# Performance work log

Measured on AMD Instinct MI355X. Metric: run time of the kernel, lower is better.

Reference implementation:

```python
import jax, jax.numpy as jnp
import numpy as np

E = 2048        # embedding_dim
H = 16          # num_q_heads
G = 4           # group_size
HKV = H // G    # num_kv_heads = 4
D = E // H      # q_head_dim = 128
KVD = E // G    # kv_head_dim = 512
B, N = 2, 2048


def setup_inputs() -> dict:
    key = jax.random.key(0)
    ks = jax.random.split(key, 5)
    s = 0.02
    return {
        "x": jax.random.normal(ks[0], (B, N, E), jnp.float32),
        "Wq": jax.random.normal(ks[1], (E, E), jnp.float32) * s,
        "Wk": jax.random.normal(ks[2], (KVD, E), jnp.float32) * s,
        "Wv": jax.random.normal(ks[3], (KVD, E), jnp.float32) * s,
        "Wo": jax.random.normal(ks[4], (E, E), jnp.float32) * s,
    }


def reference(x, Wq, Wk, Wv, Wo):
    b, n, _ = x.shape
    # projections (nn.Linear: y = x @ W.T)
    q = x @ Wq.T                              # (b, n, E)
    k = x @ Wk.T                              # (b, n, KVD)
    v = x @ Wv.T                              # (b, n, KVD)
    # split heads: q -> b h n d with h=H, then (h g) -> g,h layout
    q = q.reshape(b, n, H, D).transpose(0, 2, 1, 3)          # b H n d
    q = q.reshape(b, HKV, G, n, D).transpose(0, 2, 1, 3, 4)  # b g h n d  (h=HKV)
    k = k.reshape(b, n, HKV, D).transpose(0, 2, 1, 3)        # b h s d
    v = v.reshape(b, n, HKV, D).transpose(0, 2, 1, 3)        # b h s d
    scale = 1.0 / jnp.sqrt(jnp.asarray(D, x.dtype))
    scores = jnp.einsum('bghnd,bhsd->bghns', q, k) * scale   # full score tensor
    scores = jax.nn.softmax(scores, axis=-1)
    # dropout p=0.0 -> identity
    o = jnp.einsum('bghns,bhsd->bghnd', scores, v)           # b g h n d
    # rearrange 'b g h n d -> b n (h g) d' then concat heads
    o = o.transpose(0, 3, 2, 1, 4).reshape(b, n, E)          # b n (h g) d -> b n E
    return o @ Wo.T
```

## Files before the change

kernel.cpp:

```cpp
#include <hip/hip_runtime.h>
#include <hip/hip_bf16.h>
#include <cstdint>
#include <cstddef>

using u16 = unsigned short;
typedef __bf16 bf16x8 __attribute__((ext_vector_type(8)));
typedef float f32x4 __attribute__((ext_vector_type(4)));
typedef float f32x16 __attribute__((ext_vector_type(16)));
typedef u16 u16x4 __attribute__((ext_vector_type(4)));
typedef u16 u16x8 __attribute__((ext_vector_type(8)));
typedef uint32_t u32x4 __attribute__((ext_vector_type(4)));

__device__ __forceinline__ u16 f2bf(float f) {
  uint32_t u = __builtin_bit_cast(uint32_t, f);
  u += 0x7FFFu + ((u >> 16) & 1u);
  return (u16)(u >> 16);
}

__device__ __forceinline__ void gld_lds16(const void* g, void* l) {
  __builtin_amdgcn_global_load_lds(
      (const __attribute__((address_space(1))) unsigned int*)g,
      (__attribute__((address_space(3))) unsigned int*)l, 16, 0, 0);
}

#define MFMA16(a, b, c) __builtin_amdgcn_mfma_f32_16x16x32_bf16((a), (b), (c), 0, 0, 0)
#define MFMA32(a, b, c) __builtin_amdgcn_mfma_f32_32x32x16_bf16((a), (b), (c), 0, 0, 0)

__device__ __forceinline__ uint32_t pkbf(float a, float b) {
  uint32_t d;
  asm("v_cvt_pk_bf16_f32 %0, %1, %2" : "=v"(d) : "v"(a), "v"(b));
  return d;
}
__device__ __forceinline__ void swap32(uint32_t& a, uint32_t& b) {
  asm volatile("v_permlane32_swap_b32 %0, %1" : "+v"(a), "+v"(b));
}

__global__ void cvt_kernel(const float* __restrict__ in, u16* __restrict__ out, int n4) {
  int i = blockIdx.x * blockDim.x + threadIdx.x;
  int stride = gridDim.x * blockDim.x;
  for (; i < n4; i += stride) {
    float4 v = reinterpret_cast<const float4*>(in)[i];
    u16x4 o;
    o[0] = f2bf(v.x); o[1] = f2bf(v.y); o[2] = f2bf(v.z); o[3] = f2bf(v.w);
    reinterpret_cast<u16x4*>(out)[i] = o;
  }
}

__global__ void cvt4_kernel(const float* __restrict__ x, const float* __restrict__ Wq,
                            const float* __restrict__ Wk, const float* __restrict__ Wv,
                            u16* __restrict__ xb, u16* __restrict__ Wc) {
  int i = blockIdx.x * blockDim.x + threadIdx.x;
  int stride = gridDim.x * blockDim.x;
  for (; i < 3670016; i += stride) {
    const float* src; u16* dst; int off;
    if (i < 2097152)      { src = x;  dst = xb;            off = i; }
    else if (i < 3145728) { src = Wq; dst = Wc;            off = i - 2097152; }
    else if (i < 3407872) { src = Wk; dst = Wc + 4194304;  off = i - 3145728; }
    else                  { src = Wv; dst = Wc + 5242880;  off = i - 3407872; }
    float4 v = reinterpret_cast<const float4*>(src)[off];
    u16x4 o;
    o[0] = f2bf(v.x); o[1] = f2bf(v.y); o[2] = f2bf(v.z); o[3] = f2bf(v.w);
    reinterpret_cast<u16x4*>(dst)[off] = o;
  }
}

template <bool OUT_BF16>
__global__ __launch_bounds__(256) void gemm_bt(const u16* __restrict__ A,
                                               const u16* __restrict__ B,
                                               void* __restrict__ Cv,
                                               int M, int N, int K) {
  __shared__ __align__(16) u16 Ash[3][128 * 32];
  __shared__ __align__(16) u16 Bsh[3][128 * 32];
  const int tid = threadIdx.x;
  const int w = tid >> 6, lane = tid & 63, ql = lane & 15, g = lane >> 4;
  const int wr = w >> 1, wc = w & 1;
  const int m0 = blockIdx.y * 128, n0 = blockIdx.x * 128;
  const int srow = w * 16 + (lane >> 2);
  const int sk = (lane & 3) * 8;
  const u16* Abase = A + (size_t)(m0 + srow) * K + sk;
  const u16* Bbase = B + (size_t)(n0 + srow) * K + sk;

  f32x4 acc[4][4];
#pragma unroll
  for (int i = 0; i < 4; i++)
#pragma unroll
    for (int j = 0; j < 4; j++) acc[i][j] = f32x4{0.f, 0.f, 0.f, 0.f};

  auto stage = [&](int bi, int tile) {
    const int kt = tile * 32;
    gld_lds16(Abase + kt,                  &Ash[bi][w * 512]);
    gld_lds16(Abase + (size_t)64 * K + kt, &Ash[bi][2048 + w * 512]);
    gld_lds16(Bbase + kt,                  &Bsh[bi][w * 512]);
    gld_lds16(Bbase + (size_t)64 * K + kt, &Bsh[bi][2048 + w * 512]);
  };

  const int nt = K >> 5;
  stage(0, 0);
  stage(1, 1);
  asm volatile("s_waitcnt vmcnt(4)" ::: "memory");
  __builtin_amdgcn_sched_barrier(0);
  __builtin_amdgcn_s_barrier();
  __builtin_amdgcn_sched_barrier(0);

  int cur = 0;
  for (int t = 0; t < nt; ++t) {
    if (t + 2 < nt) {
      int stg = cur + 2; if (stg >= 3) stg -= 3;
      stage(stg, t + 2);
    }
    bf16x8 af[4], bfr[4];
#pragma unroll
    for (int i = 0; i < 4; i++)
      af[i] = *reinterpret_cast<const bf16x8*>(&Ash[cur][(wr * 64 + i * 16 + ql) * 32 + g * 8]);
#pragma unroll
    for (int j = 0; j < 4; j++)
      bfr[j] = *reinterpret_cast<const bf16x8*>(&Bsh[cur][(wc * 64 + j * 16 + ql) * 32 + g * 8]);
    __builtin_amdgcn_s_setprio(1);
#pragma unroll
    for (int i = 0; i < 4; i++)
#pragma unroll
      for (int j = 0; j < 4; j++)
        acc[i][j] = MFMA16(af[i], bfr[j], acc[i][j]);
    __builtin_amdgcn_s_setprio(0);
    if (t + 1 < nt) {
      if (t + 2 < nt) {
        asm volatile("s_waitcnt vmcnt(4)" ::: "memory");
      } else {
        asm volatile("s_waitcnt vmcnt(0)" ::: "memory");
      }
      __builtin_amdgcn_sched_barrier(0);
      __builtin_amdgcn_s_barrier();
      __builtin_amdgcn_sched_barrier(0);
    }
    cur = (cur == 2) ? 0 : cur + 1;
  }

#pragma unroll
  for (int i = 0; i < 4; i++)
#pragma unroll
    for (int j = 0; j < 4; j++)
#pragma unroll
      for (int r = 0; r < 4; r++) {
        const int row = m0 + wr * 64 + i * 16 + g * 4 + r;
        const int col = n0 + wc * 64 + j * 16 + ql;
        if constexpr (OUT_BF16)
          ((u16*)Cv)[(size_t)row * N + col] = f2bf(acc[i][j][r]);
        else
          ((float*)Cv)[(size_t)row * N + col] = acc[i][j][r];
      }
}

__global__ __launch_bounds__(256, 2) void attn_kernel(const u16* __restrict__ QKV,
                                                      u16* __restrict__ O) {
  __shared__ __align__(16) u16 Kb[2][64 * 128];
  __shared__ __align__(16) u16 Vb[3][2][128 * 32];
  const int tid = threadIdx.x, w = tid >> 6, lane = tid & 63;
  const int lq = lane & 31, hi = lane >> 5;
  const int bid = blockIdx.x;
  const int swz = (bid & 7) * 64 + (bid >> 3);
  const int qt = swz & 15;
  const int bh = swz >> 4;
  const int b = bh >> 4, h = bh & 15, hkv = h >> 2;
  const size_t rowb = (size_t)b * 2048;
  const int qbase = qt * 128 + w * 32;

  const u16* Kg = QKV + 2048 + hkv * 128;
  const u16* Vg = QKV + 2560 + hkv * 128;

  bf16x8 bq[8];
  {
    const u16* qp = QKV + (rowb + qbase + lq) * 3072 + h * 128 + hi * 8;
#pragma unroll
    for (int s5 = 0; s5 < 8; s5++)
      bq[s5] = *reinterpret_cast<const bf16x8*>(qp + s5 * 16);
  }

  const int dg = tid & 7, sl = tid >> 3;

  f32x16 oacc[4], lacc;
#pragma unroll
  for (int dt = 0; dt < 4; dt++)
#pragma unroll
    for (int i = 0; i < 16; i++) oacc[dt][i] = 0.f;
#pragma unroll
  for (int i = 0; i < 16; i++) lacc[i] = 0.f;
  float m = -INFINITY;
  const float CEXP = 0.08838834764831845f * 1.4426950408889634f;

  const bf16x8 ones = __builtin_bit_cast(bf16x8,
      u32x4{0x3F803F80u, 0x3F803F80u, 0x3F803F80u, 0x3F803F80u});

  auto stageK = [&](int pb2, int sbase) {
#pragma unroll
    for (int p = 0; p < 4; p++) {
      const int L = p * 2048 + tid * 8;
      const int s = L >> 7;
      const int gI = (L >> 3) & 15;
      gld_lds16(Kg + (rowb + sbase + s) * 3072 + ((gI ^ (s & 7)) << 3),
                &Kb[pb2][p * 2048 + w * 512]);
    }
  };
  auto writeV = [&](int vb3, const u16x8& a00, const u16x8& a01,
                    const u16x8& a10, const u16x8& a11) {
#pragma unroll
    for (int sh2 = 0; sh2 < 2; sh2++)
#pragma unroll
      for (int hf = 0; hf < 2; hf++) {
        const u16x8 v = sh2 ? (hf ? a11 : a10) : (hf ? a01 : a00);
#pragma unroll
        for (int j = 0; j < 8; j++) {
          const int d = dg * 16 + hf * 8 + j;
          const int key = ((d >> 1) ^ (d >> 4)) & 3;
          Vb[vb3][sh2][d * 32 + (sl ^ (key << 3))] = v[j];
        }
      }
  };

#define KFRAG(PB, SH, S5) \
  (*reinterpret_cast<const bf16x8*>(&Kb[PB][((SH)*32 + lq) * 128 + ((((S5)*2 + hi) ^ (lq & 7)) << 3)]))
#define VFRAG(VB, DT, SS) \
  (*reinterpret_cast<const bf16x8*>(&Vb[VB][(SS) >> 1][((DT)*32 + lq) * 32 + \
      ((((SS) & 1) * 16 + hi * 8) ^ (((((DT)*32 + lq) >> 1) ^ (((DT)*32 + lq) >> 4)) & 3) << 3)]))

  u16x8 v00, v01, v10, v11;
  {
    const u16* vp = Vg + (rowb + sl) * 3072 + dg * 16;
    v00 = *reinterpret_cast<const u16x8*>(vp);
    v01 = *reinterpret_cast<const u16x8*>(vp + 8);
    const u16* vp2 = vp + (size_t)32 * 3072;
    v10 = *reinterpret_cast<const u16x8*>(vp2);
    v11 = *reinterpret_cast<const u16x8*>(vp2 + 8);
  }
  stageK(0, 0);
  writeV(0, v00, v01, v10, v11);
  __syncthreads();

  bf16x8 pf0, pf1, pf2, pf3;
  int vprev = 2, vcur = 0, vnext = 1;

#pragma unroll 1
  for (int sb = 0; sb < 32; sb++) {
    const int pb = sb & 1;
    if (sb < 31) {
      const u16* vp = Vg + (rowb + (sb + 1) * 64 + sl) * 3072 + dg * 16;
      v00 = *reinterpret_cast<const u16x8*>(vp);
      v01 = *reinterpret_cast<const u16x8*>(vp + 8);
      const u16* vp2 = vp + (size_t)32 * 3072;
      v10 = *reinterpret_cast<const u16x8*>(vp2);
      v11 = *reinterpret_cast<const u16x8*>(vp2 + 8);
      stageK(pb ^ 1, (sb + 1) * 64);
    }

    f32x16 sc0, sc1;
#pragma unroll
    for (int i = 0; i < 16; i++) { sc0[i] = 0.f; sc1[i] = 0.f; }
    __builtin_amdgcn_s_setprio(1);
#pragma unroll
    for (int s5 = 0; s5 < 8; s5++) {
      sc0 = MFMA32(KFRAG(pb, 0, s5), bq[s5], sc0);
      sc1 = MFMA32(KFRAG(pb, 1, s5), bq[s5], sc1);
    }
    __builtin_amdgcn_s_setprio(0);

    if (sb) {
      __builtin_amdgcn_s_setprio(1);
#pragma unroll
      for (int dt = 0; dt < 4; dt++) {
        oacc[dt] = MFMA32(VFRAG(vprev, dt, 0), pf0, oacc[dt]);
        oacc[dt] = MFMA32(VFRAG(vprev, dt, 1), pf1, oacc[dt]);
        oacc[dt] = MFMA32(VFRAG(vprev, dt, 2), pf2, oacc[dt]);
        oacc[dt] = MFMA32(VFRAG(vprev, dt, 3), pf3, oacc[dt]);
      }
      __builtin_amdgcn_s_setprio(0);
    }

    float u[16];
#pragma unroll
    for (int i = 0; i < 16; i++) u[i] = fmaxf(sc0[i], sc1[i]);
#pragma unroll
    for (int i = 0; i < 8; i++) u[i] = fmaxf(u[i], u[i + 8]);
#pragma unroll
    for (int i = 0; i < 4; i++) u[i] = fmaxf(u[i], u[i + 4]);
    float mx = fmaxf(fmaxf(u[0], u[1]), fmaxf(u[2], u[3]));
    mx = fmaxf(mx, __shfl_xor(mx, 32));

    if (__any((mx - m) * CEXP > 8.0f)) {
      const float mn = fmaxf(m, mx);
      const float corr = exp2f((m - mn) * CEXP);
#pragma unroll
      for (int i = 0; i < 16; i++) lacc[i] *= corr;
#pragma unroll
      for (int dt = 0; dt < 4; dt++)
#pragma unroll
        for (int i = 0; i < 16; i++) oacc[dt][i] *= corr;
      m = mn;
    }

    const float mC = m * CEXP;
    float e0[16], e1[16];
#pragma unroll
    for (int i = 0; i < 16; i++) {
      e0[i] = exp2f(fmaf(sc0[i], CEXP, -mC));
      e1[i] = exp2f(fmaf(sc1[i], CEXP, -mC));
    }
    {
      uint32_t a, bw;
      u32x4 f;
      a = pkbf(e0[0], e0[1]);  bw = pkbf(e0[4], e0[5]);  swap32(a, bw);
      f[0] = a; f[2] = bw;
      a = pkbf(e0[2], e0[3]);  bw = pkbf(e0[6], e0[7]);  swap32(a, bw);
      f[1] = a; f[3] = bw;
      pf0 = __builtin_bit_cast(bf16x8, f);
      a = pkbf(e0[8], e0[9]);  bw = pkbf(e0[12], e0[13]); swap32(a, bw);
      f[0] = a; f[2] = bw;
      a = pkbf(e0[10], e0[11]); bw = pkbf(e0[14], e0[15]); swap32(a, bw);
      f[1] = a; f[3] = bw;
      pf1 = __builtin_bit_cast(bf16x8, f);
      a = pkbf(e1[0], e1[1]);  bw = pkbf(e1[4], e1[5]);  swap32(a, bw);
      f[0] = a; f[2] = bw;
      a = pkbf(e1[2], e1[3]);  bw = pkbf(e1[6], e1[7]);  swap32(a, bw);
      f[1] = a; f[3] = bw;
      pf2 = __builtin_bit_cast(bf16x8, f);
      a = pkbf(e1[8], e1[9]);  bw = pkbf(e1[12], e1[13]); swap32(a, bw);
      f[0] = a; f[2] = bw;
      a = pkbf(e1[10], e1[11]); bw = pkbf(e1[14], e1[15]); swap32(a, bw);
      f[1] = a; f[3] = bw;
      pf3 = __builtin_bit_cast(bf16x8, f);
    }

    lacc = MFMA32(ones, pf0, lacc);
    lacc = MFMA32(ones, pf1, lacc);
    lacc = MFMA32(ones, pf2, lacc);
    lacc = MFMA32(ones, pf3, lacc);

    if (sb < 31) writeV(vnext, v00, v01, v10, v11);
    __syncthreads();

    const int tmp = vprev; vprev = vcur; vcur = vnext; vnext = tmp;
  }

  {
    __builtin_amdgcn_s_setprio(1);
#pragma unroll
    for (int dt = 0; dt < 4; dt++) {
      oacc[dt] = MFMA32(VFRAG(vprev, dt, 0), pf0, oacc[dt]);
      oacc[dt] = MFMA32(VFRAG(vprev, dt, 1), pf1, oacc[dt]);
      oacc[dt] = MFMA32(VFRAG(vprev, dt, 2), pf2, oacc[dt]);
      oacc[dt] = MFMA32(VFRAG(vprev, dt, 3), pf3, oacc[dt]);
    }
    __builtin_amdgcn_s_setprio(0);
  }
  __syncthreads();

  const float rl = 1.0f / lacc[0];
  u16* ob = (w < 2) ? &Kb[w][0] : &Vb[w - 2][0][0];
#pragma unroll
  for (int dt = 0; dt < 4; dt++)
#pragma unroll
    for (int rq = 0; rq < 4; rq++) {
      u16x4 pv;
#pragma unroll
      for (int k = 0; k < 4; k++) pv[k] = f2bf(oacc[dt][rq * 4 + k] * rl);
      *reinterpret_cast<u16x4*>(&ob[lq * 136 + dt * 32 + rq * 8 + hi * 4]) = pv;
    }
  const int orow = lane >> 1, och = (lane & 1) * 64;
  u16* og = O + (rowb + qbase + orow) * 2048 + h * 128 + och;
#pragma unroll
  for (int t = 0; t < 8; t++) {
    u16x8 v = *reinterpret_cast<const u16x8*>(&ob[orow * 136 + och + t * 8]);
    *reinterpret_cast<u16x8*>(og + t * 8) = v;
  }
#undef KFRAG
#undef VFRAG
}

extern "C" void kernel_launch(void* const* d_in, const int* in_sizes, int n_in,
                              void* d_out, int out_size, void* d_ws, size_t ws_size,
                              hipStream_t stream) {
  (void)in_sizes; (void)n_in; (void)out_size;
  const float* x  = (const float*)d_in[0];
  const float* Wq = (const float*)d_in[1];
  const float* Wk = (const float*)d_in[2];
  const float* Wv = (const float*)d_in[3];
  const float* Wo = (const float*)d_in[4];

  if (ws_size < (size_t)(8388608 + 6291456 + 12582912) * 2) return;
  u16* xb  = (u16*)d_ws;
  u16* Wc  = xb + 8388608;
  u16* QKV = Wc + 6291456;
  u16* Ob  = xb;

  cvt4_kernel<<<2048, 256, 0, stream>>>(x, Wq, Wk, Wv, xb, Wc);
  gemm_bt<true><<<dim3(24, 32), 256, 0, stream>>>(xb, Wc, (void*)QKV, 4096, 3072, 2048);
  cvt_kernel<<<2048, 256, 0, stream>>>(Wo, Wc, 1048576);
  attn_kernel<<<dim3(512), 256, 0, stream>>>(QKV, Ob);
  gemm_bt<false><<<dim3(16, 32), 256, 0, stream>>>(Ob, Wc, d_out, 4096, 2048, 2048);
}
```

Measured before the change: 233.2 us.

## Process two query tiles per wave with 32-key blocks in attention

Each wave now owns 64 query rows, held as two 32-row MFMA tiles. Every K and V fragment read from shared memory therefore feeds two MFMAs, which halves LDS traffic per FLOP and halves the grid to 256 blocks. Key blocks shrink to 32 with plain double buffering instead of the three-stage V pipeline. The row sum is now taken with a shuffle reduction instead of an MFMA against a vector of ones. The cost is higher register pressure, fewer blocks (256 on a device with about 256 CUs), and less overlap because P·V is no longer deferred to the next iteration.

```diff
diff --git a/kernel.cpp b/kernel.cpp
--- a/kernel.cpp
+++ b/kernel.cpp
@@ -152,103 +152,86 @@
 
 __global__ __launch_bounds__(256, 2) void attn_kernel(const u16* __restrict__ QKV,
                                                       u16* __restrict__ O) {
-  __shared__ __align__(16) u16 Kb[2][64 * 128];
-  __shared__ __align__(16) u16 Vb[3][2][128 * 32];
+  __shared__ __align__(16) u16 SH[17408];
   const int tid = threadIdx.x, w = tid >> 6, lane = tid & 63;
   const int lq = lane & 31, hi = lane >> 5;
   const int bid = blockIdx.x;
-  const int swz = (bid & 7) * 64 + (bid >> 3);
-  const int qt = swz & 15;
-  const int bh = swz >> 4;
-  const int b = bh >> 4, h = bh & 15, hkv = h >> 2;
+  const int cls = bid & 7, uu = bid >> 3;
+  const int b = cls >> 2, hkv = cls & 3;
+  const int h = hkv * 4 + (uu >> 3), qt = uu & 7;
   const size_t rowb = (size_t)b * 2048;
-  const int qbase = qt * 128 + w * 32;
+  const int qbase = qt * 256 + w * 64;
 
   const u16* Kg = QKV + 2048 + hkv * 128;
   const u16* Vg = QKV + 2560 + hkv * 128;
 
-  bf16x8 bq[8];
+  bf16x8 bq0[8], bq1[8];
   {
-    const u16* qp = QKV + (rowb + qbase + lq) * 3072 + h * 128 + hi * 8;
-#pragma unroll
-    for (int s5 = 0; s5 < 8; s5++)
-      bq[s5] = *reinterpret_cast<const bf16x8*>(qp + s5 * 16);
+    const u16* qp0 = QKV + (rowb + qbase + lq) * 3072 + h * 128 + hi * 8;
+    const u16* qp1 = qp0 + (size_t)32 * 3072;
+#pragma unroll
+    for (int s5 = 0; s5 < 8; s5++) {
+      bq0[s5] = *reinterpret_cast<const bf16x8*>(qp0 + s5 * 16);
+      bq1[s5] = *reinterpret_cast<const bf16x8*>(qp1 + s5 * 16);
+    }
   }
 
   const int dg = tid & 7, sl = tid >> 3;
-
-  f32x16 oacc[4], lacc;
+  const int ks = tid >> 4, kslot = tid & 15;
+
+  f32x16 oa0[4], oa1[4];
 #pragma unroll
   for (int dt = 0; dt < 4; dt++)
 #pragma unroll
-    for (int i = 0; i < 16; i++) oacc[dt][i] = 0.f;
-#pragma unroll
-  for (int i = 0; i < 16; i++) lacc[i] = 0.f;
-  float m = -INFINITY;
+    for (int i = 0; i < 16; i++) { oa0[dt][i] = 0.f; oa1[dt][i] = 0.f; }
+  float m0 = -INFINITY, m1 = -INFINITY, l0 = 0.f, l1 = 0.f;
   const float CEXP = 0.08838834764831845f * 1.4426950408889634f;
 
-  const bf16x8 ones = __builtin_bit_cast(bf16x8,
-      u32x4{0x3F803F80u, 0x3F803F80u, 0x3F803F80u, 0x3F803F80u});
-
-  auto stageK = [&](int pb2, int sbase) {
-#pragma unroll
-    for (int p = 0; p < 4; p++) {
-      const int L = p * 2048 + tid * 8;
-      const int s = L >> 7;
-      const int gI = (L >> 3) & 15;
-      gld_lds16(Kg + (rowb + sbase + s) * 3072 + ((gI ^ (s & 7)) << 3),
-                &Kb[pb2][p * 2048 + w * 512]);
+  auto stageK = [&](int pb, int sbase) {
+#pragma unroll
+    for (int p = 0; p < 2; p++) {
+      const int s = p * 16 + ks;
+      gld_lds16(Kg + (rowb + sbase + s) * 3072 + ((kslot ^ (s & 7)) << 3),
+                &SH[pb * 4096 + p * 2048 + w * 512]);
     }
   };
-  auto writeV = [&](int vb3, const u16x8& a00, const u16x8& a01,
-                    const u16x8& a10, const u16x8& a11) {
-#pragma unroll
-    for (int sh2 = 0; sh2 < 2; sh2++)
-#pragma unroll
-      for (int hf = 0; hf < 2; hf++) {
-        const u16x8 v = sh2 ? (hf ? a11 : a10) : (hf ? a01 : a00);
-#pragma unroll
-        for (int j = 0; j < 8; j++) {
-          const int d = dg * 16 + hf * 8 + j;
-          const int key = ((d >> 1) ^ (d >> 4)) & 3;
-          Vb[vb3][sh2][d * 32 + (sl ^ (key << 3))] = v[j];
-        }
-      }
+  auto writeV = [&](int pb, const u16x8& a0, const u16x8& a1) {
+#pragma unroll
+    for (int hf = 0; hf < 2; hf++) {
+      const u16x8 v = hf ? a1 : a0;
+#pragma unroll
+      for (int j = 0; j < 8; j++) {
+        const int d = dg * 16 + hf * 8 + j;
+        const int key = ((d >> 1) ^ (d >> 4)) & 3;
+        SH[8192 + pb * 4096 + d * 32 + (sl ^ (key << 3))] = v[j];
+      }
+    }
   };
 
-#define KFRAG(PB, SH, S5) \
-  (*reinterpret_cast<const bf16x8*>(&Kb[PB][((SH)*32 + lq) * 128 + ((((S5)*2 + hi) ^ (lq & 7)) << 3)]))
-#define VFRAG(VB, DT, SS) \
-  (*reinterpret_cast<const bf16x8*>(&Vb[VB][(SS) >> 1][((DT)*32 + lq) * 32 + \
-      ((((SS) & 1) * 16 + hi * 8) ^ (((((DT)*32 + lq) >> 1) ^ (((DT)*32 + lq) >> 4)) & 3) << 3)]))
-
-  u16x8 v00, v01, v10, v11;
+#define KFRAG(PB, S5) \
+  (*reinterpret_cast<const bf16x8*>(&SH[(PB)*4096 + lq * 128 + ((((S5)*2 + hi) ^ (lq & 7)) << 3)]))
+#define VFRAG(PB, DT, SS) \
+  (*reinterpret_cast<const bf16x8*>(&SH[8192 + (PB)*4096 + ((DT)*32 + lq) * 32 + \
+      (((SS)*16 + hi * 8) ^ ((((((DT)*32 + lq) >> 1) ^ (((DT)*32 + lq) >> 4)) & 3) << 3))]))
+
+  u16x8 va, vb2;
   {
     const u16* vp = Vg + (rowb + sl) * 3072 + dg * 16;
-    v00 = *reinterpret_cast<const u16x8*>(vp);
-    v01 = *reinterpret_cast<const u16x8*>(vp + 8);
-    const u16* vp2 = vp + (size_t)32 * 3072;
-    v10 = *reinterpret_cast<const u16x8*>(vp2);
-    v11 = *reinterpret_cast<const u16x8*>(vp2 + 8);
+    va  = *reinterpret_cast<const u16x8*>(vp);
+    vb2 = *reinterpret_cast<const u16x8*>(vp + 8);
   }
   stageK(0, 0);
-  writeV(0, v00, v01, v10, v11);
+  writeV(0, va, vb2);
   __syncthreads();
 
-  bf16x8 pf0, pf1, pf2, pf3;
-  int vprev = 2, vcur = 0, vnext = 1;
-
 #pragma unroll 1
-  for (int sb = 0; sb < 32; sb++) {
+  for (int sb = 0; sb < 64; sb++) {
     const int pb = sb & 1;
-    if (sb < 31) {
-      const u16* vp = Vg + (rowb + (sb + 1) * 64 + sl) * 3072 + dg * 16;
-      v00 = *reinterpret_cast<const u16x8*>(vp);
-      v01 = *reinterpret_cast<const u16x8*>(vp + 8);
-      const u16* vp2 = vp + (size_t)32 * 3072;
-      v10 = *reinterpret_cast<const u16x8*>(vp2);
-      v11 = *reinterpret_cast<const u16x8*>(vp2 + 8);
-      stageK(pb ^ 1, (sb + 1) * 64);
+    if (sb < 63) {
+      const u16* vp = Vg + (rowb + (sb + 1) * 32 + sl) * 3072 + dg * 16;
+      va  = *reinterpret_cast<const u16x8*>(vp);
+      vb2 = *reinterpret_cast<const u16x8*>(vp + 8);
+      stageK(pb ^ 1, (sb + 1) * 32);
     }
 
     f32x16 sc0, sc1;
@@ -257,118 +240,150 @@
     __builtin_amdgcn_s_setprio(1);
 #pragma unroll
     for (int s5 = 0; s5 < 8; s5++) {
-      sc0 = MFMA32(KFRAG(pb, 0, s5), bq[s5], sc0);
-      sc1 = MFMA32(KFRAG(pb, 1, s5), bq[s5], sc1);
+      bf16x8 kf = KFRAG(pb, s5);
+      sc0 = MFMA32(kf, bq0[s5], sc0);
+      sc1 = MFMA32(kf, bq1[s5], sc1);
     }
     __builtin_amdgcn_s_setprio(0);
 
-    if (sb) {
-      __builtin_amdgcn_s_setprio(1);
-#pragma unroll
-      for (int dt = 0; dt < 4; dt++) {
-        oacc[dt] = MFMA32(VFRAG(vprev, dt, 0), pf0, oacc[dt]);
-        oacc[dt] = MFMA32(VFRAG(vprev, dt, 1), pf1, oacc[dt]);
-        oacc[dt] = MFMA32(VFRAG(vprev, dt, 2), pf2, oacc[dt]);
-        oacc[dt] = MFMA32(VFRAG(vprev, dt, 3), pf3, oacc[dt]);
-      }
-      __builtin_amdgcn_s_setprio(0);
-    }
-
-    float u[16];
-#pragma unroll
-    for (int i = 0; i < 16; i++) u[i] = fmaxf(sc0[i], sc1[i]);
-#pragma unroll
-    for (int i = 0; i < 8; i++) u[i] = fmaxf(u[i], u[i + 8]);
-#pragma unroll
-    for (int i = 0; i < 4; i++) u[i] = fmaxf(u[i], u[i + 4]);
-    float mx = fmaxf(fmaxf(u[0], u[1]), fmaxf(u[2], u[3]));
-    mx = fmaxf(mx, __shfl_xor(mx, 32));
-
-    if (__any((mx - m) * CEXP > 8.0f)) {
-      const float mn = fmaxf(m, mx);
-      const float corr = exp2f((m - mn) * CEXP);
-#pragma unroll
-      for (int i = 0; i < 16; i++) lacc[i] *= corr;
-#pragma unroll
-      for (int dt = 0; dt < 4; dt++)
-#pragma unroll
-        for (int i = 0; i < 16; i++) oacc[dt][i] *= corr;
-      m = mn;
-    }
-
-    const float mC = m * CEXP;
-    float e0[16], e1[16];
-#pragma unroll
-    for (int i = 0; i < 16; i++) {
-      e0[i] = exp2f(fmaf(sc0[i], CEXP, -mC));
-      e1[i] = exp2f(fmaf(sc1[i], CEXP, -mC));
-    }
+    bf16x8 pf00, pf01, pf10, pf11;
+
     {
-      uint32_t a, bw;
-      u32x4 f;
-      a = pkbf(e0[0], e0[1]);  bw = pkbf(e0[4], e0[5]);  swap32(a, bw);
+      float u[8];
+#pragma unroll
+      for (int i = 0; i < 8; i++) u[i] = fmaxf(sc0[i], sc0[i + 8]);
+#pragma unroll
+      for (int i = 0; i < 4; i++) u[i] = fmaxf(u[i], u[i + 4]);
+      float mx = fmaxf(fmaxf(u[0], u[1]), fmaxf(u[2], u[3]));
+      mx = fmaxf(mx, __shfl_xor(mx, 32));
+      if (__any((mx - m0) * CEXP > 8.0f)) {
+        const float mn = fmaxf(m0, mx);
+        const float corr = exp2f((m0 - mn) * CEXP);
+        l0 *= corr;
+#pragma unroll
+        for (int dt = 0; dt < 4; dt++)
+#pragma unroll
+          for (int i = 0; i < 16; i++) oa0[dt][i] *= corr;
+        m0 = mn;
+      }
+      const float mC = m0 * CEXP;
+#pragma unroll
+      for (int i = 0; i < 16; i++) sc0[i] = exp2f(fmaf(sc0[i], CEXP, -mC));
+      float s[8];
+#pragma unroll
+      for (int i = 0; i < 8; i++) s[i] = sc0[i] + sc0[i + 8];
+#pragma unroll
+      for (int i = 0; i < 4; i++) s[i] = s[i] + s[i + 4];
+      float ps = (s[0] + s[1]) + (s[2] + s[3]);
+      ps += __shfl_xor(ps, 32);
+      l0 += ps;
+      uint32_t a, bw; u32x4 f;
+      a = pkbf(sc0[0], sc0[1]);   bw = pkbf(sc0[4], sc0[5]);   swap32(a, bw);
       f[0] = a; f[2] = bw;
-      a = pkbf(e0[2], e0[3]);  bw = pkbf(e0[6], e0[7]);  swap32(a, bw);
+      a = pkbf(sc0[2], sc0[3]);   bw = pkbf(sc0[6], sc0[7]);   swap32(a, bw);
       f[1] = a; f[3] = bw;
-      pf0 = __builtin_bit_cast(bf16x8, f);
-      a = pkbf(e0[8], e0[9]);  bw = pkbf(e0[12], e0[13]); swap32(a, bw);
+      pf00 = __builtin_bit_cast(bf16x8, f);
+      a = pkbf(sc0[8], sc0[9]);   bw = pkbf(sc0[12], sc0[13]); swap32(a, bw);
       f[0] = a; f[2] = bw;
-      a = pkbf(e0[10], e0[11]); bw = pkbf(e0[14], e0[15]); swap32(a, bw);
+      a = pkbf(sc0[10], sc0[11]); bw = pkbf(sc0[14], sc0[15]); swap32(a, bw);
       f[1] = a; f[3] = bw;
-      pf1 = __builtin_bit_cast(bf16x8, f);
-      a = pkbf(e1[0], e1[1]);  bw = pkbf(e1[4], e1[5]);  swap32(a, bw);
+      pf01 = __builtin_bit_cast(bf16x8, f);
+    }
+    {
+      float u[8];
+#pragma unroll
+      for (int i = 0; i < 8; i++) u[i] = fmaxf(sc1[i], sc1[i + 8]);
+#pragma unroll
+      for (int i = 0; i < 4; i++) u[i] = fmaxf(u[i], u[i + 4]);
+      float mx = fmaxf(fmaxf(u[0], u[1]), fmaxf(u[2], u[3]));
+      mx = fmaxf(mx, __shfl_xor(mx, 32));
+      if (__any((mx - m1) * CEXP > 8.0f)) {
+        const float mn = fmaxf(m1, mx);
+        const float corr = exp2f((m1 - mn) * CEXP);
+        l1 *= corr;
+#pragma unroll
+        for (int dt = 0; dt < 4; dt++)
+#pragma unroll
+          for (int i = 0; i < 16; i++) oa1[dt][i] *= corr;
+        m1 = mn;
+      }
+      const float mC = m1 * CEXP;
+#pragma unroll
+      for (int i = 0; i < 16; i++) sc1[i] = exp2f(fmaf(sc1[i], CEXP, -mC));
+      float s[8];
+#pragma unroll
+      for (int i = 0; i < 8; i++) s[i] = sc1[i] + sc1[i + 8];
+#pragma unroll
+      for (int i = 0; i < 4; i++) s[i] = s[i] + s[i + 4];
+      float ps = (s[0] + s[1]) + (s[2] + s[3]);
+      ps += __shfl_xor(ps, 32);
+      l1 += ps;
+      uint32_t a, bw; u32x4 f;
+      a = pkbf(sc1[0], sc1[1]);   bw = pkbf(sc1[4], sc1[5]);   swap32(a, bw);
       f[0] = a; f[2] = bw;
-      a = pkbf(e1[2], e1[3]);  bw = pkbf(e1[6], e1[7]);  swap32(a, bw);
+      a = pkbf(sc1[2], sc1[3]);   bw = pkbf(sc1[6], sc1[7]);   swap32(a, bw);
       f[1] = a; f[3] = bw;
-      pf2 = __builtin_bit_cast(bf16x8, f);
-      a = pkbf(e1[8], e1[9]);  bw = pkbf(e1[12], e1[13]); swap32(a, bw);
+      pf10 = __builtin_bit_cast(bf16x8, f);
+      a = pkbf(sc1[8], sc1[9]);   bw = pkbf(sc1[12], sc1[13]); swap32(a, bw);
       f[0] = a; f[2] = bw;
-      a = pkbf(e1[10], e1[11]); bw = pkbf(e1[14], e1[15]); swap32(a, bw);
+      a = pkbf(sc1[10], sc1[11]); bw = pkbf(sc1[14], sc1[15]); swap32(a, bw);
       f[1] = a; f[3] = bw;
-      pf3 = __builtin_bit_cast(bf16x8, f);
-    }
-
-    lacc = MFMA32(ones, pf0, lacc);
-    lacc = MFMA32(ones, pf1, lacc);
-    lacc = MFMA32(ones, pf2, lacc);
-    lacc = MFMA32(ones, pf3, lacc);
-
-    if (sb < 31) writeV(vnext, v00, v01, v10, v11);
+      pf11 = __builtin_bit_cast(bf16x8, f);
+    }
+
+    __builtin_amdgcn_s_setprio(1);
+#pragma unroll
+    for (int dt = 0; dt < 4; dt++) {
+      bf16x8 vf0 = VFRAG(pb, dt, 0);
+      oa0[dt] = MFMA32(vf0, pf00, oa0[dt]);
+      oa1[dt] = MFMA32(vf0, pf10, oa1[dt]);
+      bf16x8 vf1 = VFRAG(pb, dt, 1);
+      oa0[dt] = MFMA32(vf1, pf01, oa0[dt]);
+      oa1[dt] = MFMA32(vf1, pf11, oa1[dt]);
+    }
+    __builtin_amdgcn_s_setprio(0);
+
+    if (sb < 63) writeV(pb ^ 1, va, vb2);
     __syncthreads();
-
-    const int tmp = vprev; vprev = vcur; vcur = vnext; vnext = tmp;
-  }
-
+  }
+
+  u16* ob = SH + w * 4352;
+  const int orow = lane >> 1, och = (lane & 1) * 64;
   {
-    __builtin_amdgcn_s_setprio(1);
-#pragma unroll
-    for (int dt = 0; dt < 4; dt++) {
-      oacc[dt] = MFMA32(VFRAG(vprev, dt, 0), pf0, oacc[dt]);
-      oacc[dt] = MFMA32(VFRAG(vprev, dt, 1), pf1, oacc[dt]);
-      oacc[dt] = MFMA32(VFRAG(vprev, dt, 2), pf2, oacc[dt]);
-      oacc[dt] = MFMA32(VFRAG(vprev, dt, 3), pf3, oacc[dt]);
-    }
-    __builtin_amdgcn_s_setprio(0);
-  }
-  __syncthreads();
-
-  const float rl = 1.0f / lacc[0];
-  u16* ob = (w < 2) ? &Kb[w][0] : &Vb[w - 2][0][0];
-#pragma unroll
-  for (int dt = 0; dt < 4; dt++)
-#pragma unroll
-    for (int rq = 0; rq < 4; rq++) {
-      u16x4 pv;
-#pragma unroll
-      for (int k = 0; k < 4; k++) pv[k] = f2bf(oacc[dt][rq * 4 + k] * rl);
-      *reinterpret_cast<u16x4*>(&ob[lq * 136 + dt * 32 + rq * 8 + hi * 4]) = pv;
-    }
-  const int orow = lane >> 1, och = (lane & 1) * 64;
-  u16* og = O + (rowb + qbase + orow) * 2048 + h * 128 + och;
-#pragma unroll
-  for (int t = 0; t < 8; t++) {
-    u16x8 v = *reinterpret_cast<const u16x8*>(&ob[orow * 136 + och + t * 8]);
-    *reinterpret_cast<u16x8*>(og + t * 8) = v;
+    const float rl = 1.0f / l0;
+#pragma unroll
+    for (int dt = 0; dt < 4; dt++)
+#pragma unroll
+      for (int rq = 0; rq < 4; rq++) {
+        u16x4 pv;
+#pragma unroll
+        for (int k = 0; k < 4; k++) pv[k] = f2bf(oa0[dt][rq * 4 + k] * rl);
+        *reinterpret_cast<u16x4*>(&ob[lq * 136 + dt * 32 + rq * 8 + hi * 4]) = pv;
+      }
+    u16* og = O + (rowb + qbase + orow) * 2048 + h * 128 + och;
+#pragma unroll
+    for (int t = 0; t < 8; t++) {
+      u16x8 v = *reinterpret_cast<const u16x8*>(&ob[orow * 136 + och + t * 8]);
+      *reinterpret_cast<u16x8*>(og + t * 8) = v;
+    }
+  }
+  {
+    const float rl = 1.0f / l1;
+#pragma unroll
+    for (int dt = 0; dt < 4; dt++)
+#pragma unroll
+      for (int rq = 0; rq < 4; rq++) {
+        u16x4 pv;
+#pragma unroll
+        for (int k = 0; k < 4; k++) pv[k] = f2bf(oa1[dt][rq * 4 + k] * rl);
+        *reinterpret_cast<u16x4*>(&ob[lq * 136 + dt * 32 + rq * 8 + hi * 4]) = pv;
+      }
+    u16* og = O + (rowb + qbase + 32 + orow) * 2048 + h * 128 + och;
+#pragma unroll
+    for (int t = 0; t < 8; t++) {
+      u16x8 v = *reinterpret_cast<const u16x8*>(&ob[orow * 136 + och + t * 8]);
+      *reinterpret_cast<u16x8*>(og + t * 8) = v;
+    }
   }
 #undef KFRAG
 #undef VFRAG
@@ -393,6 +408,6 @@
   cvt4_kernel<<<2048, 256, 0, stream>>>(x, Wq, Wk, Wv, xb, Wc);
   gemm_bt<true><<<dim3(24, 32), 256, 0, stream>>>(xb, Wc, (void*)QKV, 4096, 3072, 2048);
   cvt_kernel<<<2048, 256, 0, stream>>>(Wo, Wc, 1048576);
-  attn_kernel<<<dim3(512), 256, 0, stream>>>(QKV, Ob);
+  attn_kernel<<<dim3(256), 256, 0, stream>>>(QKV, Ob);
   gemm_bt<false><<<dim3(16, 32), 256, 0, stream>>>(Ob, Wc, d_out, 4096, 2048, 2048);
 }
```

Measured after the change: 374.3 us. +60.5%, slower.

## Switch projection GEMM to 32x32 MFMA tiles with XOR-swizzled LDS layout

Applied to the files above, without the earlier changes.

The bf16 GEMM used for the QKV and output projections now issues 32x32x16 MFMA instructions on 2x2 fragments per wave instead of 16x16 MFMAs on 4x4 fragments. This reduces the number of LDS fragment reads and MFMA issues per k-tile. The 16-byte chunks in LDS are XOR-swizzled by row so the new 32-row fragment reads avoid bank conflicts. The epilogue row mapping is updated to match the 32x32 accumulator layout. It relies on an MFMA32 macro that must exist elsewhere in the file.

```diff
diff --git a/kernel.cpp b/kernel.cpp
--- a/kernel.cpp
+++ b/kernel.cpp
@@ -72,19 +72,22 @@
   __shared__ __align__(16) u16 Ash[3][128 * 32];
   __shared__ __align__(16) u16 Bsh[3][128 * 32];
   const int tid = threadIdx.x;
-  const int w = tid >> 6, lane = tid & 63, ql = lane & 15, g = lane >> 4;
+  const int w = tid >> 6, lane = tid & 63;
+  const int lq = lane & 31, hi = lane >> 5;
   const int wr = w >> 1, wc = w & 1;
   const int m0 = blockIdx.y * 128, n0 = blockIdx.x * 128;
   const int srow = w * 16 + (lane >> 2);
-  const int sk = (lane & 3) * 8;
+  const int sk = ((lane & 3) ^ (srow & 3)) * 8;
   const u16* Abase = A + (size_t)(m0 + srow) * K + sk;
   const u16* Bbase = B + (size_t)(n0 + srow) * K + sk;
 
-  f32x4 acc[4][4];
-#pragma unroll
-  for (int i = 0; i < 4; i++)
-#pragma unroll
-    for (int j = 0; j < 4; j++) acc[i][j] = f32x4{0.f, 0.f, 0.f, 0.f};
+  f32x16 acc[2][2];
+#pragma unroll
+  for (int i = 0; i < 2; i++)
+#pragma unroll
+    for (int j = 0; j < 2; j++)
+#pragma unroll
+      for (int r = 0; r < 16; r++) acc[i][j][r] = 0.f;
 
   auto stage = [&](int bi, int tile) {
     const int kt = tile * 32;
@@ -94,6 +97,11 @@
     gld_lds16(Bbase + (size_t)64 * K + kt, &Bsh[bi][2048 + w * 512]);
   };
 
+#define AFRAG(BUF, I, T) \
+  (*reinterpret_cast<const bf16x8*>(&Ash[BUF][(wr * 64 + (I) * 32 + lq) * 32 + ((((T) * 2 + hi) ^ (lq & 3)) * 8)]))
+#define BFRAG(BUF, J, T) \
+  (*reinterpret_cast<const bf16x8*>(&Bsh[BUF][(wc * 64 + (J) * 32 + lq) * 32 + ((((T) * 2 + hi) ^ (lq & 3)) * 8)]))
+
   const int nt = K >> 5;
   stage(0, 0);
   stage(1, 1);
@@ -108,19 +116,22 @@
       int stg = cur + 2; if (stg >= 3) stg -= 3;
       stage(stg, t + 2);
     }
-    bf16x8 af[4], bfr[4];
-#pragma unroll
-    for (int i = 0; i < 4; i++)
-      af[i] = *reinterpret_cast<const bf16x8*>(&Ash[cur][(wr * 64 + i * 16 + ql) * 32 + g * 8]);
-#pragma unroll
-    for (int j = 0; j < 4; j++)
-      bfr[j] = *reinterpret_cast<const bf16x8*>(&Bsh[cur][(wc * 64 + j * 16 + ql) * 32 + g * 8]);
+    bf16x8 af[2][2], bfv[2][2];
+#pragma unroll
+    for (int i = 0; i < 2; i++)
+#pragma unroll
+      for (int kk = 0; kk < 2; kk++) {
+        af[i][kk]  = AFRAG(cur, i, kk);
+        bfv[i][kk] = BFRAG(cur, i, kk);
+      }
     __builtin_amdgcn_s_setprio(1);
 #pragma unroll
-    for (int i = 0; i < 4; i++)
-#pragma unroll
-      for (int j = 0; j < 4; j++)
-        acc[i][j] = MFMA16(af[i], bfr[j], acc[i][j]);
+    for (int i = 0; i < 2; i++)
+#pragma unroll
+      for (int j = 0; j < 2; j++)
+#pragma unroll
+        for (int kk = 0; kk < 2; kk++)
+          acc[i][j] = MFMA32(af[i][kk], bfv[j][kk], acc[i][j]);
     __builtin_amdgcn_s_setprio(0);
     if (t + 1 < nt) {
       if (t + 2 < nt) {
@@ -136,18 +147,20 @@
   }
 
 #pragma unroll
-  for (int i = 0; i < 4; i++)
-#pragma unroll
-    for (int j = 0; j < 4; j++)
-#pragma unroll
-      for (int r = 0; r < 4; r++) {
-        const int row = m0 + wr * 64 + i * 16 + g * 4 + r;
-        const int col = n0 + wc * 64 + j * 16 + ql;
+  for (int i = 0; i < 2; i++)
+#pragma unroll
+    for (int j = 0; j < 2; j++)
+#pragma unroll
+      for (int r = 0; r < 16; r++) {
+        const int row = m0 + wr * 64 + i * 32 + (r & 3) + 8 * (r >> 2) + 4 * hi;
+        const int col = n0 + wc * 64 + j * 32 + lq;
         if constexpr (OUT_BF16)
           ((u16*)Cv)[(size_t)row * N + col] = f2bf(acc[i][j][r]);
         else
           ((float*)Cv)[(size_t)row * N + col] = acc[i][j][r];
       }
+#undef AFRAG
+#undef BFRAG
 }
 
 __global__ __launch_bounds__(256, 2) void attn_kernel(const u16* __restrict__ QKV,
```

After: 256.8 us. +10.1%, slower.

## Split attention over two KV halves with a separate combine kernel

Applied to the files above, without the earlier changes.

The attention kernel now splits the key/value sequence into two halves (split-K flash decoding style). The grid doubles to 1024 blocks, each using a 32-key tile and smaller shared memory, and launch bounds rise to allow 4 blocks per CU. Each block writes a bf16 partial output plus its per-row max and sum, and a new combine kernel rescales and merges the two partials. This adds parallelism and occupancy, at the cost of extra global traffic for the partials, an extra kernel launch, and double bf16 rounding of the output.

```diff
diff --git a/kernel.cpp b/kernel.cpp
--- a/kernel.cpp
+++ b/kernel.cpp
@@ -15,6 +15,10 @@
   uint32_t u = __builtin_bit_cast(uint32_t, f);
   u += 0x7FFFu + ((u >> 16) & 1u);
   return (u16)(u >> 16);
+}
+__device__ __forceinline__ float bf2f(u16 h) {
+  uint32_t u = ((uint32_t)h) << 16;
+  return __builtin_bit_cast(float, u);
 }
 
 __device__ __forceinline__ void gld_lds16(const void* g, void* l) {
@@ -150,19 +154,20 @@
       }
 }
 
-__global__ __launch_bounds__(256, 2) void attn_kernel(const u16* __restrict__ QKV,
-                                                      u16* __restrict__ O) {
-  __shared__ __align__(16) u16 Kb[2][64 * 128];
-  __shared__ __align__(16) u16 Vb[3][2][128 * 32];
+__global__ __launch_bounds__(256, 4) void attn_kernel(const u16* __restrict__ QKV,
+                                                      u16* __restrict__ Op,
+                                                      float* __restrict__ ml) {
+  __shared__ __align__(16) u16 SH[20480];
   const int tid = threadIdx.x, w = tid >> 6, lane = tid & 63;
   const int lq = lane & 31, hi = lane >> 5;
   const int bid = blockIdx.x;
-  const int swz = (bid & 7) * 64 + (bid >> 3);
-  const int qt = swz & 15;
-  const int bh = swz >> 4;
-  const int b = bh >> 4, h = bh & 15, hkv = h >> 2;
+  const int cls = bid & 7, uu = bid >> 3;
+  const int b = cls >> 2, hkv = cls & 3;
+  const int kvh = uu & 1, qt = (uu >> 1) & 15, hsub = uu >> 5;
+  const int h = hkv * 4 + hsub;
   const size_t rowb = (size_t)b * 2048;
   const int qbase = qt * 128 + w * 32;
+  const int sb0 = kvh * 1024;
 
   const u16* Kg = QKV + 2048 + hkv * 128;
   const u16* Vg = QKV + 2560 + hkv * 128;
@@ -190,76 +195,65 @@
   const bf16x8 ones = __builtin_bit_cast(bf16x8,
       u32x4{0x3F803F80u, 0x3F803F80u, 0x3F803F80u, 0x3F803F80u});
 
-  auto stageK = [&](int pb2, int sbase) {
-#pragma unroll
-    for (int p = 0; p < 4; p++) {
+  auto stageK = [&](int pb, int sbase) {
+#pragma unroll
+    for (int p = 0; p < 2; p++) {
       const int L = p * 2048 + tid * 8;
       const int s = L >> 7;
       const int gI = (L >> 3) & 15;
       gld_lds16(Kg + (rowb + sbase + s) * 3072 + ((gI ^ (s & 7)) << 3),
-                &Kb[pb2][p * 2048 + w * 512]);
+                &SH[pb * 4096 + p * 2048 + w * 512]);
     }
   };
-  auto writeV = [&](int vb3, const u16x8& a00, const u16x8& a01,
-                    const u16x8& a10, const u16x8& a11) {
-#pragma unroll
-    for (int sh2 = 0; sh2 < 2; sh2++)
-#pragma unroll
-      for (int hf = 0; hf < 2; hf++) {
-        const u16x8 v = sh2 ? (hf ? a11 : a10) : (hf ? a01 : a00);
-#pragma unroll
-        for (int j = 0; j < 8; j++) {
-          const int d = dg * 16 + hf * 8 + j;
-          const int key = ((d >> 1) ^ (d >> 4)) & 3;
-          Vb[vb3][sh2][d * 32 + (sl ^ (key << 3))] = v[j];
-        }
+  auto writeV = [&](int vb3, const u16x8& a0, const u16x8& a1) {
+#pragma unroll
+    for (int hf = 0; hf < 2; hf++) {
+      const u16x8 v = hf ? a1 : a0;
+#pragma unroll
+      for (int j = 0; j < 8; j++) {
+        const int d = dg * 16 + hf * 8 + j;
+        const int key = ((d >> 1) ^ (d >> 4)) & 3;
+        SH[8192 + vb3 * 4096 + d * 32 + (sl ^ (key << 3))] = v[j];
       }
+    }
   };
 
-#define KFRAG(PB, SH, S5) \
-  (*reinterpret_cast<const bf16x8*>(&Kb[PB][((SH)*32 + lq) * 128 + ((((S5)*2 + hi) ^ (lq & 7)) << 3)]))
+#define KFRAG(PB, S5) \
+  (*reinterpret_cast<const bf16x8*>(&SH[(PB)*4096 + lq * 128 + ((((S5)*2 + hi) ^ (lq & 7)) << 3)]))
 #define VFRAG(VB, DT, SS) \
-  (*reinterpret_cast<const bf16x8*>(&Vb[VB][(SS) >> 1][((DT)*32 + lq) * 32 + \
-      ((((SS) & 1) * 16 + hi * 8) ^ (((((DT)*32 + lq) >> 1) ^ (((DT)*32 + lq) >> 4)) & 3) << 3)]))
-
-  u16x8 v00, v01, v10, v11;
+  (*reinterpret_cast<const bf16x8*>(&SH[8192 + (VB)*4096 + ((DT)*32 + lq) * 32 + \
+      (((SS)*16 + hi * 8) ^ ((((((DT)*32 + lq) >> 1) ^ (((DT)*32 + lq) >> 4)) & 3) << 3))]))
+
+  u16x8 va, vb2;
   {
-    const u16* vp = Vg + (rowb + sl) * 3072 + dg * 16;
-    v00 = *reinterpret_cast<const u16x8*>(vp);
-    v01 = *reinterpret_cast<const u16x8*>(vp + 8);
-    const u16* vp2 = vp + (size_t)32 * 3072;
-    v10 = *reinterpret_cast<const u16x8*>(vp2);
-    v11 = *reinterpret_cast<const u16x8*>(vp2 + 8);
-  }
-  stageK(0, 0);
-  writeV(0, v00, v01, v10, v11);
+    const u16* vp = Vg + (rowb + sb0 + sl) * 3072 + dg * 16;
+    va  = *reinterpret_cast<const u16x8*>(vp);
+    vb2 = *reinterpret_cast<const u16x8*>(vp + 8);
+  }
+  stageK(0, sb0);
+  writeV(0, va, vb2);
   __syncthreads();
 
-  bf16x8 pf0, pf1, pf2, pf3;
+  bf16x8 pf0, pf1;
   int vprev = 2, vcur = 0, vnext = 1;
 
 #pragma unroll 1
   for (int sb = 0; sb < 32; sb++) {
     const int pb = sb & 1;
     if (sb < 31) {
-      const u16* vp = Vg + (rowb + (sb + 1) * 64 + sl) * 3072 + dg * 16;
-      v00 = *reinterpret_cast<const u16x8*>(vp);
-      v01 = *reinterpret_cast<const u16x8*>(vp + 8);
-      const u16* vp2 = vp + (size_t)32 * 3072;
-      v10 = *reinterpret_cast<const u16x8*>(vp2);
-      v11 = *reinterpret_cast<const u16x8*>(vp2 + 8);
-      stageK(pb ^ 1, (sb + 1) * 64);
-    }
-
-    f32x16 sc0, sc1;
-#pragma unroll
-    for (int i = 0; i < 16; i++) { sc0[i] = 0.f; sc1[i] = 0.f; }
+      const u16* vp = Vg + (rowb + sb0 + (sb + 1) * 32 + sl) * 3072 + dg * 16;
+      va  = *reinterpret_cast<const u16x8*>(vp);
+      vb2 = *reinterpret_cast<const u16x8*>(vp + 8);
+      stageK(pb ^ 1, sb0 + (sb + 1) * 32);
+    }
+
+    f32x16 sc;
+#pragma unroll
+    for (int i = 0; i < 16; i++) sc[i] = 0.f;
     __builtin_amdgcn_s_setprio(1);
 #pragma unroll
-    for (int s5 = 0; s5 < 8; s5++) {
-      sc0 = MFMA32(KFRAG(pb, 0, s5), bq[s5], sc0);
-      sc1 = MFMA32(KFRAG(pb, 1, s5), bq[s5], sc1);
-    }
+    for (int s5 = 0; s5 < 8; s5++)
+      sc = MFMA32(KFRAG(pb, s5), bq[s5], sc);
     __builtin_amdgcn_s_setprio(0);
 
     if (sb) {
@@ -268,17 +262,13 @@
       for (int dt = 0; dt < 4; dt++) {
         oacc[dt] = MFMA32(VFRAG(vprev, dt, 0), pf0, oacc[dt]);
         oacc[dt] = MFMA32(VFRAG(vprev, dt, 1), pf1, oacc[dt]);
-        oacc[dt] = MFMA32(VFRAG(vprev, dt, 2), pf2, oacc[dt]);
-        oacc[dt] = MFMA32(VFRAG(vprev, dt, 3), pf3, oacc[dt]);
       }
       __builtin_amdgcn_s_setprio(0);
     }
 
-    float u[16];
-#pragma unroll
-    for (int i = 0; i < 16; i++) u[i] = fmaxf(sc0[i], sc1[i]);
-#pragma unroll
-    for (int i = 0; i < 8; i++) u[i] = fmaxf(u[i], u[i + 8]);
+    float u[8];
+#pragma unroll
+    for (int i = 0; i < 8; i++) u[i] = fmaxf(sc[i], sc[i + 8]);
 #pragma unroll
     for (int i = 0; i < 4; i++) u[i] = fmaxf(u[i], u[i + 4]);
     float mx = fmaxf(fmaxf(u[0], u[1]), fmaxf(u[2], u[3]));
@@ -297,43 +287,28 @@
     }
 
     const float mC = m * CEXP;
-    float e0[16], e1[16];
-#pragma unroll
-    for (int i = 0; i < 16; i++) {
-      e0[i] = exp2f(fmaf(sc0[i], CEXP, -mC));
-      e1[i] = exp2f(fmaf(sc1[i], CEXP, -mC));
-    }
+    float e[16];
+#pragma unroll
+    for (int i = 0; i < 16; i++) e[i] = exp2f(fmaf(sc[i], CEXP, -mC));
     {
       uint32_t a, bw;
       u32x4 f;
-      a = pkbf(e0[0], e0[1]);  bw = pkbf(e0[4], e0[5]);  swap32(a, bw);
+      a = pkbf(e[0], e[1]);   bw = pkbf(e[4], e[5]);   swap32(a, bw);
       f[0] = a; f[2] = bw;
-      a = pkbf(e0[2], e0[3]);  bw = pkbf(e0[6], e0[7]);  swap32(a, bw);
+      a = pkbf(e[2], e[3]);   bw = pkbf(e[6], e[7]);   swap32(a, bw);
       f[1] = a; f[3] = bw;
       pf0 = __builtin_bit_cast(bf16x8, f);
-      a = pkbf(e0[8], e0[9]);  bw = pkbf(e0[12], e0[13]); swap32(a, bw);
+      a = pkbf(e[8], e[9]);   bw = pkbf(e[12], e[13]); swap32(a, bw);
       f[0] = a; f[2] = bw;
-      a = pkbf(e0[10], e0[11]); bw = pkbf(e0[14], e0[15]); swap32(a, bw);
+      a = pkbf(e[10], e[11]); bw = pkbf(e[14], e[15]); swap32(a, bw);
       f[1] = a; f[3] = bw;
       pf1 = __builtin_bit_cast(bf16x8, f);
-      a = pkbf(e1[0], e1[1]);  bw = pkbf(e1[4], e1[5]);  swap32(a, bw);
-      f[0] = a; f[2] = bw;
-      a = pkbf(e1[2], e1[3]);  bw = pkbf(e1[6], e1[7]);  swap32(a, bw);
-      f[1] = a; f[3] = bw;
-      pf2 = __builtin_bit_cast(bf16x8, f);
-      a = pkbf(e1[8], e1[9]);  bw = pkbf(e1[12], e1[13]); swap32(a, bw);
-      f[0] = a; f[2] = bw;
-      a = pkbf(e1[10], e1[11]); bw = pkbf(e1[14], e1[15]); swap32(a, bw);
-      f[1] = a; f[3] = bw;
-      pf3 = __builtin_bit_cast(bf16x8, f);
     }
 
     lacc = MFMA32(ones, pf0, lacc);
     lacc = MFMA32(ones, pf1, lacc);
-    lacc = MFMA32(ones, pf2, lacc);
-    lacc = MFMA32(ones, pf3, lacc);
-
-    if (sb < 31) writeV(vnext, v00, v01, v10, v11);
+
+    if (sb < 31) writeV(vnext, va, vb2);
     __syncthreads();
 
     const int tmp = vprev; vprev = vcur; vcur = vnext; vnext = tmp;
@@ -345,15 +320,14 @@
     for (int dt = 0; dt < 4; dt++) {
       oacc[dt] = MFMA32(VFRAG(vprev, dt, 0), pf0, oacc[dt]);
       oacc[dt] = MFMA32(VFRAG(vprev, dt, 1), pf1, oacc[dt]);
-      oacc[dt] = MFMA32(VFRAG(vprev, dt, 2), pf2, oacc[dt]);
-      oacc[dt] = MFMA32(VFRAG(vprev, dt, 3), pf3, oacc[dt]);
     }
     __builtin_amdgcn_s_setprio(0);
   }
   __syncthreads();
 
-  const float rl = 1.0f / lacc[0];
-  u16* ob = (w < 2) ? &Kb[w][0] : &Vb[w - 2][0][0];
+  const float lsum = lacc[0];
+  const float rl = 1.0f / lsum;
+  u16* ob = SH + w * 4352;
 #pragma unroll
   for (int dt = 0; dt < 4; dt++)
 #pragma unroll
@@ -363,8 +337,13 @@
       for (int k = 0; k < 4; k++) pv[k] = f2bf(oacc[dt][rq * 4 + k] * rl);
       *reinterpret_cast<u16x4*>(&ob[lq * 136 + dt * 32 + rq * 8 + hi * 4]) = pv;
     }
+  if (hi == 0) {
+    const int idx = (b * 16 + h) * 2048 + qbase + lq;
+    *reinterpret_cast<float2*>(&ml[(size_t)kvh * 131072 + idx * 2]) = float2{m, lsum};
+  }
+  __builtin_amdgcn_s_barrier();
   const int orow = lane >> 1, och = (lane & 1) * 64;
-  u16* og = O + (rowb + qbase + orow) * 2048 + h * 128 + och;
+  u16* og = Op + (size_t)kvh * 8388608 + (rowb + qbase + orow) * 2048 + h * 128 + och;
 #pragma unroll
   for (int t = 0; t < 8; t++) {
     u16x8 v = *reinterpret_cast<const u16x8*>(&ob[orow * 136 + och + t * 8]);
@@ -372,6 +351,34 @@
   }
 #undef KFRAG
 #undef VFRAG
+}
+
+__global__ void combine_kernel(const u16* __restrict__ Op, const float* __restrict__ ml,
+                               u16* __restrict__ Ob) {
+  const float CEXP = 0.08838834764831845f * 1.4426950408889634f;
+  int i = blockIdx.x * blockDim.x + threadIdx.x;
+  const int stride = gridDim.x * blockDim.x;
+  for (; i < 1048576; i += stride) {
+    const int r = i >> 8;
+    const int c8 = i & 255;
+    const int bb = r >> 11, q = r & 2047, hh = c8 >> 4;
+    const int idx = (bb * 16 + hh) * 2048 + q;
+    float2 ml1 = *reinterpret_cast<const float2*>(&ml[idx * 2]);
+    float2 ml2 = *reinterpret_cast<const float2*>(&ml[131072 + idx * 2]);
+    const float mm = fmaxf(ml1.x, ml2.x);
+    const float w1 = exp2f((ml1.x - mm) * CEXP) * ml1.y;
+    const float w2 = exp2f((ml2.x - mm) * CEXP) * ml2.y;
+    const float inv = 1.0f / (w1 + w2);
+    const float f1 = w1 * inv, f2 = w2 * inv;
+    const size_t off = (size_t)r * 2048 + c8 * 8;
+    u16x8 v1 = *reinterpret_cast<const u16x8*>(Op + off);
+    u16x8 v2 = *reinterpret_cast<const u16x8*>(Op + 8388608 + off);
+    u16x8 o;
+#pragma unroll
+    for (int j = 0; j < 8; j++)
+      o[j] = f2bf(f1 * bf2f(v1[j]) + f2 * bf2f(v2[j]));
+    *reinterpret_cast<u16x8*>(Ob + off) = o;
+  }
 }
 
 extern "C" void kernel_launch(void* const* d_in, const int* in_sizes, int n_in,
@@ -389,10 +396,13 @@
   u16* Wc  = xb + 8388608;
   u16* QKV = Wc + 6291456;
   u16* Ob  = xb;
+  u16* Op  = (u16*)d_out;
+  float* ml = (float*)(Wc + 4194304);
 
   cvt4_kernel<<<2048, 256, 0, stream>>>(x, Wq, Wk, Wv, xb, Wc);
   gemm_bt<true><<<dim3(24, 32), 256, 0, stream>>>(xb, Wc, (void*)QKV, 4096, 3072, 2048);
   cvt_kernel<<<2048, 256, 0, stream>>>(Wo, Wc, 1048576);
-  attn_kernel<<<dim3(512), 256, 0, stream>>>(QKV, Ob);
+  attn_kernel<<<dim3(1024), 256, 0, stream>>>(QKV, Op, ml);
+  combine_kernel<<<dim3(2048), 256, 0, stream>>>(Op, ml, Ob);
   gemm_bt<false><<<dim3(16, 32), 256, 0, stream>>>(Ob, Wc, d_out, 4096, 2048, 2048);
 }
```

After: 487.2 us. +108.9%, slower.
